# Performance work log

Measured on AMD Instinct MI355X. Metric: run time of the kernel, lower is better.

## Reference

```python
import jax, jax.numpy as jnp
import numpy as np

K = 16
TAU = 1.0
EPS = np.float32(np.finfo(np.float32).tiny)
B, N = 2048, 16384


def setup_inputs() -> dict:
    key = jax.random.key(0)
    k1, k2 = jax.random.split(key)
    scores = jax.random.normal(k1, (B, N), dtype=jnp.float32)
    # Gumbel(0,1) noise, materialized explicitly for determinism
    u = jax.random.uniform(k2, (B, N), dtype=jnp.float32, minval=1e-7, maxval=1.0 - 1e-7)
    g = -jnp.log(-jnp.log(u))
    return {"scores": scores, "g": g}


def reference(scores, g):
    # perturbed scores
    s = scores + g
    khot = jnp.zeros_like(s)
    onehot = jnp.zeros_like(s)

    def step(carry, _):
        s, khot, onehot = carry
        khot_mask = jnp.maximum(1.0 - onehot, EPS)          # [B, N]
        s = s + jnp.log(khot_mask)
        onehot = jax.nn.softmax(s / TAU, axis=1)            # row-wise softmax
        khot = khot + onehot
        return (s, khot, onehot), None

    (_, khot, _), _ = jax.lax.scan(step, (s, khot, onehot), None, length=K)
    return khot  # hard=False -> relaxed k-hot vector
```

## Files before the change

kernel.cpp:

```cpp
#include <hip/hip_runtime.h>
#include <math.h>


#define N_COLS   16384
#define K_ITERS  16
#define NTHREADS 1024
#define EPT      (N_COLS / NTHREADS)
#define V4       (EPT / 4)

__global__ __launch_bounds__(NTHREADS, 4)
void subset_topk_kernel(const float* __restrict__ scores,
                        const float* __restrict__ g,
                        float* __restrict__ out)
{
    __shared__ float red[2][16];

    const int tid  = threadIdx.x;
    const int lane = tid & 63;
    const int wid  = tid >> 6;
    const size_t base = (size_t)blockIdx.x * N_COLS;

    const float4* s4 = (const float4*)(scores + base);
    const float4* g4 = (const float4*)(g + base);
    float4*       o4 = (float4*)(out + base);

    float e[EPT], khot[EPT];
    float zloc = 0.f;

    #pragma unroll
    for (int j = 0; j < V4; ++j) {
        float4 a = s4[j * NTHREADS + tid];
        float4 b = g4[j * NTHREADS + tid];
        float e0 = __expf(a.x + b.x);
        float e1 = __expf(a.y + b.y);
        float e2 = __expf(a.z + b.z);
        float e3 = __expf(a.w + b.w);
        e[j*4+0] = e0; e[j*4+1] = e1; e[j*4+2] = e2; e[j*4+3] = e3;
        zloc += (e0 + e1) + (e2 + e3);
        khot[j*4+0] = 0.f; khot[j*4+1] = 0.f;
        khot[j*4+2] = 0.f; khot[j*4+3] = 0.f;
    }

    #pragma unroll 1
    for (int it = 0; it < K_ITERS; ++it) {
        float z = zloc;
        #pragma unroll
        for (int o = 32; o > 0; o >>= 1) z += __shfl_xor(z, o, 64);
        if (lane == 0) red[it & 1][wid] = z;
        __syncthreads();

        float v = red[it & 1][lane & 15];
        #pragma unroll
        for (int o = 1; o < 16; o <<= 1) v += __shfl_xor(v, o, 64);

        const float inv = __builtin_amdgcn_rcpf(v);

        zloc = 0.f;
        #pragma unroll
        for (int j = 0; j < EPT; ++j) {
            float t = e[j] * inv;
            khot[j] += t;
            float en = fmaf(-t, e[j], e[j]);
            e[j] = en;
            zloc += en;
        }
    }

    #pragma unroll
    for (int j = 0; j < V4; ++j) {
        float4 r;
        r.x = khot[j*4+0]; r.y = khot[j*4+1];
        r.z = khot[j*4+2]; r.w = khot[j*4+3];
        o4[j * NTHREADS + tid] = r;
    }
}

extern "C" void kernel_launch(void* const* d_in, const int* in_sizes, int n_in,
                              void* d_out, int out_size, void* d_ws, size_t ws_size,
                              hipStream_t stream) {
    const float* scores = (const float*)d_in[0];
    const float* g      = (const float*)d_in[1];
    float* out          = (float*)d_out;

    const int rows = in_sizes[0] / N_COLS;
    subset_topk_kernel<<<rows, NTHREADS, 0, stream>>>(scores, g, out);
}
```

Measured before the change: 336.7 us.

## Fuse two softmax iterations per block reduction using sum of squares

Each reduction now gathers both the sum and the sum of squares of the current weights, so the second normalizer of a pair can be computed algebraically (Z2 = Z1 - sum(e^2)/Z1). This halves the number of block-wide reductions and barriers across the 16 iterations. Block size drops to 512 threads, which doubles the per-thread element count and register use. Computing Z2 by subtraction may introduce cancellation error when a few elements dominate.

```diff
diff --git a/kernel.cpp b/kernel.cpp
--- a/kernel.cpp
+++ b/kernel.cpp
@@ -4,16 +4,17 @@
 
 #define N_COLS   16384
 #define K_ITERS  16
-#define NTHREADS 1024
+#define NPAIRS   (K_ITERS / 2)
+#define NTHREADS 512
 #define EPT      (N_COLS / NTHREADS)
 #define V4       (EPT / 4)
 
-__global__ __launch_bounds__(NTHREADS, 4)
+__global__ __launch_bounds__(NTHREADS, 2)
 void subset_topk_kernel(const float* __restrict__ scores,
                         const float* __restrict__ g,
                         float* __restrict__ out)
 {
-    __shared__ float red[2][16];
+    __shared__ float2 red[2][8];
 
     const int tid  = threadIdx.x;
     const int lane = tid & 63;
@@ -25,8 +26,8 @@
     float4*       o4 = (float4*)(out + base);
 
     float e[EPT], khot[EPT];
-    float zloc = 0.f;
 
+    float s1a = 0.f, s1b = 0.f, s2a = 0.f, s2b = 0.f;
     #pragma unroll
     for (int j = 0; j < V4; ++j) {
         float4 a = s4[j * NTHREADS + tid];
@@ -36,33 +37,60 @@
         float e2 = __expf(a.z + b.z);
         float e3 = __expf(a.w + b.w);
         e[j*4+0] = e0; e[j*4+1] = e1; e[j*4+2] = e2; e[j*4+3] = e3;
-        zloc += (e0 + e1) + (e2 + e3);
+        s1a += e0 + e1;  s1b += e2 + e3;
+        s2a = fmaf(e0, e0, s2a); s2b = fmaf(e1, e1, s2b);
+        s2a = fmaf(e2, e2, s2a); s2b = fmaf(e3, e3, s2b);
         khot[j*4+0] = 0.f; khot[j*4+1] = 0.f;
         khot[j*4+2] = 0.f; khot[j*4+3] = 0.f;
     }
 
     #pragma unroll 1
-    for (int it = 0; it < K_ITERS; ++it) {
-        float z = zloc;
+    for (int p = 0; p < NPAIRS; ++p) {
+        float za = s1a + s1b;
+        float zb = s2a + s2b;
         #pragma unroll
-        for (int o = 32; o > 0; o >>= 1) z += __shfl_xor(z, o, 64);
-        if (lane == 0) red[it & 1][wid] = z;
+        for (int o = 32; o > 0; o >>= 1) {
+            za += __shfl_xor(za, o, 64);
+            zb += __shfl_xor(zb, o, 64);
+        }
+        if (lane == 0) red[p & 1][wid] = make_float2(za, zb);
         __syncthreads();
 
-        float v = red[it & 1][lane & 15];
+        float2 v = red[p & 1][lane & 7];
+        float va = v.x, vb = v.y;
         #pragma unroll
-        for (int o = 1; o < 16; o <<= 1) v += __shfl_xor(v, o, 64);
+        for (int o = 1; o < 8; o <<= 1) {
+            va += __shfl_xor(va, o, 64);
+            vb += __shfl_xor(vb, o, 64);
+        }
 
-        const float inv = __builtin_amdgcn_rcpf(v);
+        const float Z1   = va;
+        const float inv1 = __builtin_amdgcn_rcpf(Z1);
+        const float Z2   = fmaf(-vb, inv1, Z1);
+        const float inv2 = __builtin_amdgcn_rcpf(Z2);
 
-        zloc = 0.f;
+        s1a = 0.f; s1b = 0.f; s2a = 0.f; s2b = 0.f;
         #pragma unroll
-        for (int j = 0; j < EPT; ++j) {
-            float t = e[j] * inv;
-            khot[j] += t;
-            float en = fmaf(-t, e[j], e[j]);
-            e[j] = en;
-            zloc += en;
+        for (int j = 0; j < EPT; j += 2) {
+            float x0 = e[j+0];
+            float t0 = x0 * inv1;
+            float k0 = khot[j+0] + t0;
+            float y0 = fmaf(-t0, x0, x0);
+            float u0 = y0 * inv2;
+            khot[j+0] = k0 + u0;
+            float w0 = fmaf(-u0, y0, y0);
+            e[j+0] = w0;
+            s1a += w0; s2a = fmaf(w0, w0, s2a);
+
+            float x1 = e[j+1];
+            float t1 = x1 * inv1;
+            float k1 = khot[j+1] + t1;
+            float y1 = fmaf(-t1, x1, x1);
+            float u1 = y1 * inv2;
+            khot[j+1] = k1 + u1;
+            float w1 = fmaf(-u1, y1, y1);
+            e[j+1] = w1;
+            s1b += w1; s2b = fmaf(w1, w1, s2b);
         }
     }
 
```

Result: faster. 322.2 us (-4.3%).
